# Optimization experiments

Measured on AMD Instinct MI355X. Metric: run time of the kernel, lower is better.

## Reference

```python
import jax, jax.numpy as jnp
import numpy as np

B, S, H = 4, 2048, 1024
E, F = 8, 4096
K = 2  # hardcoded top-k in the original forward


def setup_inputs() -> dict:
    key = jax.random.key(0)
    ks = jax.random.split(key, 8)
    scale = 0.02
    x = jax.random.normal(ks[0], (B, S, H), dtype=jnp.float32)
    Wr = jax.random.normal(ks[1], (H, E), dtype=jnp.float32) * scale
    br = jnp.zeros((E,), dtype=jnp.float32)
    W1 = jax.random.normal(ks[2], (E, H, F), dtype=jnp.float32) * scale
    b1 = jnp.zeros((E, F), dtype=jnp.float32)
    W2 = jax.random.normal(ks[3], (E, F, H), dtype=jnp.float32) * scale
    b2 = jnp.zeros((E, H), dtype=jnp.float32)
    return {"x": x, "Wr": Wr, "br": br, "W1": W1, "b1": b1, "W2": W2, "b2": b2}


def reference(x, Wr, br, W1, b1, W2, b2):
    # Router: [B,S,H] @ [H,E] -> [B,S,E]
    router_logits = jnp.einsum('bsh,he->bse', x, Wr) + br
    router_probs = jax.nn.softmax(router_logits, axis=-1)
    top_k_probs, top_k_indices = jax.lax.top_k(router_probs, K)
    top_k_probs = top_k_probs / jnp.sum(top_k_probs, axis=-1, keepdims=True)
    # NOTE: original code weights EVERY selected expert by the normalized top-1 prob.
    p0 = top_k_probs[..., 0]  # [B,S]

    combined = jnp.zeros((B, S, H), dtype=x.dtype)
    for e in range(E):
        mask = jnp.any(top_k_indices == e, axis=-1)  # [B,S]
        # Dense FFN (dropout deterministic => identity); gelu approximate (flax default)
        h = jax.nn.gelu(jnp.einsum('bsh,hf->bsf', x, W1[e]) + b1[e])
        y = jnp.einsum('bsf,fh->bsh', h, W2[e]) + b2[e]
        combined = combined + jnp.where(mask[..., None], y * p0[..., None], 0.0)
    return combined
```

## Files before the change

### kernel.cpp

```cpp
#include <hip/hip_runtime.h>
#include <hip/hip_bf16.h>


typedef __bf16 bf16;
typedef __attribute__((ext_vector_type(4))) __bf16 bf16x4;
typedef __attribute__((ext_vector_type(8))) __bf16 bf16x8;
typedef __attribute__((ext_vector_type(4))) float f32x4;

#define GLD16(g, l) __builtin_amdgcn_global_load_lds( \
    (__attribute__((address_space(1))) void*)(g),      \
    (__attribute__((address_space(3))) void*)(l), 16, 0, 0)

__device__ __forceinline__ float gelu_fast(float v) {
  float u = v * fmaf(v * v, 0.0713548162726f, 1.5957691216057308f);
  return v * __builtin_amdgcn_rcpf(1.0f + __expf(-u));
}

__global__ __launch_bounds__(256) void router_kernel(
    const float* __restrict__ x, const float* __restrict__ Wr,
    const float* __restrict__ br, int* __restrict__ e01,
    float* __restrict__ p0arr) {
  int wv = threadIdx.x >> 6;
  int l = threadIdx.x & 63;
  int t = blockIdx.x * 4 + wv;
  float acc[8];
#pragma unroll
  for (int e = 0; e < 8; e++) acc[e] = 0.f;
  const float* xr = x + (size_t)t * 1024;
#pragma unroll
  for (int i = 0; i < 16; i++) {
    int h = l + i * 64;
    float xv = xr[h];
    const float4* w4 = (const float4*)(Wr + h * 8);
    float4 wa = w4[0], wb = w4[1];
    acc[0] += xv * wa.x; acc[1] += xv * wa.y; acc[2] += xv * wa.z; acc[3] += xv * wa.w;
    acc[4] += xv * wb.x; acc[5] += xv * wb.y; acc[6] += xv * wb.z; acc[7] += xv * wb.w;
  }
#pragma unroll
  for (int e = 0; e < 8; e++) {
    float v = acc[e];
#pragma unroll
    for (int m = 1; m < 64; m <<= 1) v += __shfl_xor(v, m, 64);
    acc[e] = v + br[e];
  }
  int i1 = 0; float m1 = acc[0];
#pragma unroll
  for (int e = 1; e < 8; e++) { if (acc[e] > m1) { m1 = acc[e]; i1 = e; } }
  int i2 = -1; float m2 = -3.4e38f;
#pragma unroll
  for (int e = 0; e < 8; e++) { if (e != i1 && acc[e] > m2) { m2 = acc[e]; i2 = e; } }
  if (l == 0) {
    e01[t] = i1 | (i2 << 8);
    p0arr[t] = 1.0f / (1.0f + __expf(m2 - m1));
  }
}

__global__ __launch_bounds__(1024) void slots_kernel(
    const int* __restrict__ e01, int* __restrict__ meta,
    int* __restrict__ slot1, int* __restrict__ slot2) {
  __shared__ int wtot[16];
  int tid = threadIdx.x;
  int l = tid & 63, wv = tid >> 6;
  int t0 = tid * 8;
  int i1[8], i2[8];
#pragma unroll
  for (int i = 0; i < 8; i++) {
    int ee = e01[t0 + i];
    i1[i] = ee & 255;
    i2[i] = (ee >> 8) & 255;
  }
  int offl[9];
  int running = 0;
  for (int e = 0; e < 8; e++) {
    offl[e] = running;
    int cthread = 0;
#pragma unroll
    for (int i = 0; i < 8; i++) cthread += (i1[i] == e) + (i2[i] == e);
    int inc = cthread;
#pragma unroll
    for (int d = 1; d < 64; d <<= 1) {
      int v = __shfl_up(inc, d, 64);
      if (l >= d) inc += v;
    }
    if (l == 63) wtot[wv] = inc;
    __syncthreads();
    int wbase = 0, total = 0;
#pragma unroll
    for (int w = 0; w < 16; w++) {
      int tw = wtot[w];
      wbase += (w < wv) ? tw : 0;
      total += tw;
    }
    int base = running + wbase + (inc - cthread);
#pragma unroll
    for (int i = 0; i < 8; i++) {
      if (i1[i] == e) { slot1[t0 + i] = base; base++; }
      if (i2[i] == e) { slot2[t0 + i] = base; base++; }
    }
    running += total;
    __syncthreads();
  }
  offl[8] = running;
  if (tid == 0) {
#pragma unroll
    for (int e = 0; e < 9; e++) meta[e] = offl[e];
    int nt = 0;
    for (int e = 0; e < 8; e++)
      for (int r = offl[e]; r < offl[e + 1]; r += 256)
        meta[16 + (nt++)] = r | (e << 20);
    meta[10] = nt;
  }
}

__global__ __launch_bounds__(256) void gather_kernel(
    const float* __restrict__ x, const int* __restrict__ slot1,
    const int* __restrict__ slot2, bf16* __restrict__ Xg) {
  int t = blockIdx.x;
  int s1 = slot1[t], s2 = slot2[t];
  float4 v = ((const float4*)(x + (size_t)t * 1024))[threadIdx.x];
  bf16x4 bv = { (bf16)v.x, (bf16)v.y, (bf16)v.z, (bf16)v.w };
  *(bf16x4*)(Xg + (size_t)s1 * 1024 + threadIdx.x * 4) = bv;
  *(bf16x4*)(Xg + (size_t)s2 * 1024 + threadIdx.x * 4) = bv;
}

__global__ __launch_bounds__(256) void tconv_kernel(
    const float* __restrict__ in, bf16* __restrict__ out, int R, int C) {
  __shared__ float tile[64][65];
  size_t base = (size_t)blockIdx.z * R * C;
  int gr0 = blockIdx.y * 64, gc0 = blockIdx.x * 64;
#pragma unroll
  for (int i = 0; i < 16; i++) {
    int idx = threadIdx.x + i * 256;
    int r = idx >> 6, c = idx & 63;
    tile[r][c] = in[base + (size_t)(gr0 + r) * C + gc0 + c];
  }
  __syncthreads();
  int rr0 = (threadIdx.x & 15) * 4;
#pragma unroll
  for (int i = 0; i < 4; i++) {
    int cc = (threadIdx.x >> 4) + i * 16;
    bf16x4 v = { (bf16)tile[rr0][cc], (bf16)tile[rr0 + 1][cc],
                 (bf16)tile[rr0 + 2][cc], (bf16)tile[rr0 + 3][cc] };
    *(bf16x4*)&out[base + (size_t)(gc0 + cc) * R + gr0 + rr0] = v;
  }
}

__device__ __forceinline__ void gemm256_core(
    const bf16* __restrict__ Abase, const bf16* __restrict__ Bbase,
    int K, int NT, char* smem, f32x4 acc[8][4], int wr, int wc, int l) {
  int tid = threadIdx.x;
  size_t K2 = (size_t)K * 2;
  const char* src[4];
  int dst[4];
#pragma unroll
  for (int i = 0; i < 4; i++) {
    int s = (i & 1) ? (tid + 512) : tid;
    int byteoff = s * 16;
    int p = byteoff >> 7;
    int W = byteoff & 127;
    int L = W ^ ((p & 7) << 4);
    int r = 2 * p + (L >> 6);
    int c = L & 63;
    const char* base = (const char*)((i >= 2) ? Bbase : Abase);
    src[i] = base + (size_t)r * K2 + c;
    dst[i] = ((i >= 2) ? 16384 : 0) + byteoff;
  }
  int offA[8], offB[4];
  int kc16 = (l >> 4) << 4;
#pragma unroll
  for (int mf = 0; mf < 8; mf++) {
    int r = wr * 128 + mf * 16 + (l & 15);
    int p = r >> 1;
    offA[mf] = (p << 7) + ((((r & 1) << 6) | kc16) ^ ((p & 7) << 4));
  }
#pragma unroll
  for (int nf = 0; nf < 4; nf++) {
    int r = wc * 64 + nf * 16 + (l & 15);
    int p = r >> 1;
    offB[nf] = 16384 + (p << 7) + ((((r & 1) << 6) | kc16) ^ ((p & 7) << 4));
  }
#pragma unroll
  for (int t = 0; t < 3; t++) {
    char* bu = smem + t * 32768;
#pragma unroll
    for (int i = 0; i < 4; i++) GLD16(src[i] + t * 64, bu + dst[i]);
  }
  asm volatile("s_waitcnt vmcnt(8)" ::: "memory");
  __builtin_amdgcn_s_barrier();
  for (int t = 0; t < NT; t++) {
    char* bc = smem + (t & 3) * 32768;
    char* bs = smem + ((t + 3) & 3) * 32768;
    bool st = (t + 3) < NT;
    bf16x8 bfr[4], af[4];
#pragma unroll
    for (int nf = 0; nf < 4; nf++) bfr[nf] = *(const bf16x8*)(bc + offB[nf]);
#pragma unroll
    for (int mf = 0; mf < 4; mf++) af[mf] = *(const bf16x8*)(bc + offA[mf]);
    if (st) {
      GLD16(src[0] + (t + 3) * 64, bs + dst[0]);
      GLD16(src[1] + (t + 3) * 64, bs + dst[1]);
    }
    __builtin_amdgcn_s_barrier();
    asm volatile("s_waitcnt lgkmcnt(0)" ::: "memory");
    __builtin_amdgcn_s_setprio(1);
#pragma unroll
    for (int mf = 0; mf < 4; mf++)
#pragma unroll
      for (int nf = 0; nf < 4; nf++)
        acc[mf][nf] = __builtin_amdgcn_mfma_f32_16x16x32_bf16(bfr[nf], af[mf], acc[mf][nf], 0, 0, 0);
    __builtin_amdgcn_s_setprio(0);
    __builtin_amdgcn_s_barrier();
#pragma unroll
    for (int mf = 0; mf < 4; mf++) af[mf] = *(const bf16x8*)(bc + offA[mf + 4]);
    if (st) {
      GLD16(src[2] + (t + 3) * 64, bs + dst[2]);
      GLD16(src[3] + (t + 3) * 64, bs + dst[3]);
    }
    __builtin_amdgcn_s_barrier();
    asm volatile("s_waitcnt lgkmcnt(0)" ::: "memory");
    __builtin_amdgcn_s_setprio(1);
#pragma unroll
    for (int mf = 0; mf < 4; mf++)
#pragma unroll
      for (int nf = 0; nf < 4; nf++)
        acc[mf + 4][nf] = __builtin_amdgcn_mfma_f32_16x16x32_bf16(bfr[nf], af[mf], acc[mf + 4][nf], 0, 0, 0);
    __builtin_amdgcn_s_setprio(0);
    if ((t + 3) < NT)      { asm volatile("s_waitcnt vmcnt(8)" ::: "memory"); }
    else if ((t + 2) < NT) { asm volatile("s_waitcnt vmcnt(4)" ::: "memory"); }
    else if ((t + 1) < NT) { asm volatile("s_waitcnt vmcnt(0)" ::: "memory"); }
    __builtin_amdgcn_s_barrier();
  }
}

__global__ __launch_bounds__(512, 2) void gemm1_kernel(
    const bf16* __restrict__ Xg, const bf16* __restrict__ W1t,
    const float* __restrict__ b1, bf16* __restrict__ hbuf,
    const int* __restrict__ meta) {
  __shared__ __align__(16) char smem[131072];
  int b = blockIdx.x;
  int xcd = b & 7, j = b >> 3;
  int m_idx = (j >> 4) * 8 + xcd;
  int n_tile = j & 15;
  if (m_idx >= meta[10]) return;
  int ti = meta[16 + m_idx];
  int row0 = ti & 0xFFFFF;
  int e = ti >> 20;
  int rowEnd = meta[1 + e];
  int tid = threadIdx.x;
  int w = tid >> 6, l = tid & 63;
  int wr = w >> 2, wc = w & 3;
  f32x4 acc[8][4];
#pragma unroll
  for (int a = 0; a < 8; a++)
#pragma unroll
    for (int bb = 0; bb < 4; bb++) acc[a][bb] = (f32x4){0.f, 0.f, 0.f, 0.f};
  gemm256_core(Xg + (size_t)row0 * 1024,
               W1t + ((size_t)e * 4096 + n_tile * 256) * 1024,
               1024, 32, smem, acc, wr, wc, l);
  int mrow = l & 15, nq = (l >> 4) * 4;
  int gn0 = n_tile * 256 + wc * 64 + nq;
  f32x4 bv[4];
#pragma unroll
  for (int nf = 0; nf < 4; nf++)
    bv[nf] = *(const f32x4*)(b1 + e * 4096 + gn0 + nf * 16);
#pragma unroll
  for (int mf = 0; mf < 8; mf++) {
    int gm = row0 + wr * 128 + mf * 16 + mrow;
    if (gm < rowEnd) {
      bf16* rp = hbuf + (size_t)gm * 4096 + gn0;
#pragma unroll
      for (int nf = 0; nf < 4; nf++) {
        bf16x4 o;
#pragma unroll
        for (int jj = 0; jj < 4; jj++)
          o[jj] = (bf16)gelu_fast(acc[mf][nf][jj] + bv[nf][jj]);
        *(bf16x4*)(rp + nf * 16) = o;
      }
    }
  }
}

__global__ __launch_bounds__(512, 2) void gemm2_kernel(
    const bf16* __restrict__ hbuf, const bf16* __restrict__ W2t,
    const float* __restrict__ b2, bf16* __restrict__ yb,
    const int* __restrict__ meta) {
  __shared__ __align__(16) char smem[131072];
  int b = blockIdx.x;
  int xcd = b & 7, j = b >> 3;
  int m_idx = (j >> 2) * 8 + xcd;
  int n_tile = j & 3;
  if (m_idx >= meta[10]) return;
  int ti = meta[16 + m_idx];
  int row0 = ti & 0xFFFFF;
  int e = ti >> 20;
  int rowEnd = meta[1 + e];
  int tid = threadIdx.x;
  int w = tid >> 6, l = tid & 63;
  int wr = w >> 2, wc = w & 3;
  f32x4 acc[8][4];
#pragma unroll
  for (int a = 0; a < 8; a++)
#pragma unroll
    for (int bb = 0; bb < 4; bb++) acc[a][bb] = (f32x4){0.f, 0.f, 0.f, 0.f};
  gemm256_core(hbuf + (size_t)row0 * 4096,
               W2t + ((size_t)e * 1024 + n_tile * 256) * 4096,
               4096, 128, smem, acc, wr, wc, l);
  int mrow = l & 15, nq = (l >> 4) * 4;
  int gn0 = n_tile * 256 + wc * 64 + nq;
  f32x4 bv[4];
#pragma unroll
  for (int nf = 0; nf < 4; nf++)
    bv[nf] = *(const f32x4*)(b2 + e * 1024 + gn0 + nf * 16);
#pragma unroll
  for (int mf = 0; mf < 8; mf++) {
    int gm = row0 + wr * 128 + mf * 16 + mrow;
    if (gm < rowEnd) {
      bf16* rp = yb + (size_t)gm * 1024 + gn0;
#pragma unroll
      for (int nf = 0; nf < 4; nf++) {
        bf16x4 o;
#pragma unroll
        for (int jj = 0; jj < 4; jj++)
          o[jj] = (bf16)(acc[mf][nf][jj] + bv[nf][jj]);
        *(bf16x4*)(rp + nf * 16) = o;
      }
    }
  }
}

__global__ __launch_bounds__(256) void combine_kernel(
    const bf16* __restrict__ yb, const int* __restrict__ slot1,
    const int* __restrict__ slot2, const float* __restrict__ p0arr,
    float* __restrict__ out) {
  int t = blockIdx.x;
  int s1 = slot1[t], s2 = slot2[t];
  float w0 = p0arr[t];
  bf16x4 a = *(const bf16x4*)(yb + (size_t)s1 * 1024 + threadIdx.x * 4);
  bf16x4 b = *(const bf16x4*)(yb + (size_t)s2 * 1024 + threadIdx.x * 4);
  float4 o;
  o.x = w0 * ((float)a[0] + (float)b[0]);
  o.y = w0 * ((float)a[1] + (float)b[1]);
  o.z = w0 * ((float)a[2] + (float)b[2]);
  o.w = w0 * ((float)a[3] + (float)b[3]);
  *(float4*)(out + (size_t)t * 1024 + threadIdx.x * 4) = o;
}

extern "C" void kernel_launch(void* const* d_in, const int* in_sizes, int n_in,
                              void* d_out, int out_size, void* d_ws, size_t ws_size,
                              hipStream_t stream) {
  const float* x  = (const float*)d_in[0];
  const float* Wr = (const float*)d_in[1];
  const float* br = (const float*)d_in[2];
  const float* W1 = (const float*)d_in[3];
  const float* b1 = (const float*)d_in[4];
  const float* W2 = (const float*)d_in[5];
  const float* b2 = (const float*)d_in[6];
  float* out = (float*)d_out;

  char* ws = (char*)d_ws;
  int*   meta  = (int*)(ws + 0);
  int*   e01   = (int*)(ws + 4096);
  float* p0    = (float*)(ws + 36864);
  int*   slot1 = (int*)(ws + 69632);
  int*   slot2 = (int*)(ws + 102400);
  bf16*  Xg    = (bf16*)(ws + 135168);
  bf16*  W1t   = (bf16*)(ws + 34213888ULL);
  bf16*  W2t   = (bf16*)(ws + 101322752ULL);
  bf16*  hb    = (bf16*)(ws + 168431616ULL);
  bf16*  yb    = Xg;

  tconv_kernel<<<dim3(64, 16, 8), 256, 0, stream>>>(W1, W1t, 1024, 4096);
  tconv_kernel<<<dim3(16, 64, 8), 256, 0, stream>>>(W2, W2t, 4096, 1024);
  router_kernel<<<2048, 256, 0, stream>>>(x, Wr, br, e01, p0);
  slots_kernel<<<1, 1024, 0, stream>>>(e01, meta, slot1, slot2);
  gather_kernel<<<8192, 256, 0, stream>>>(x, slot1, slot2, Xg);
  gemm1_kernel<<<1152, 512, 0, stream>>>(Xg, W1t, b1, hb, meta);
  gemm2_kernel<<<288, 512, 0, stream>>>(hb, W2t, b2, yb, meta);
  combine_kernel<<<8192, 256, 0, stream>>>(yb, slot1, slot2, p0, out);
}
```

Baseline: 792.6 us.

## Vectorize weight transpose-convert and remap GEMM tiles contiguously per XCD

The fp32-to-bf16 transpose kernel now reads with float4 loads and writes 8-wide bf16 vectors instead of scalar reads and 4-wide writes, which cuts memory instructions. The GEMM block-to-tile mapping also changes. Each XCD now gets a contiguous range of (m,n) tiles, so blocks that share the same A rows and expert weights run on the same XCD and can share its L2, and the count of live tiles is balanced across XCDs. This changes cache locality and load balance but adds a little index arithmetic. If the grid size still assumes the old layout, some blocks may exit early.

```diff
diff --git a/kernel.cpp b/kernel.cpp
--- a/kernel.cpp
+++ b/kernel.cpp
@@ -128,21 +128,40 @@
   __shared__ float tile[64][65];
   size_t base = (size_t)blockIdx.z * R * C;
   int gr0 = blockIdx.y * 64, gc0 = blockIdx.x * 64;
-#pragma unroll
-  for (int i = 0; i < 16; i++) {
-    int idx = threadIdx.x + i * 256;
-    int r = idx >> 6, c = idx & 63;
-    tile[r][c] = in[base + (size_t)(gr0 + r) * C + gc0 + c];
+  int tr = threadIdx.x >> 4;
+  int tc4 = (threadIdx.x & 15) * 4;
+#pragma unroll
+  for (int i = 0; i < 4; i++) {
+    int r = tr + i * 16;
+    float4 v = *(const float4*)&in[base + (size_t)(gr0 + r) * C + gc0 + tc4];
+    tile[r][tc4] = v.x; tile[r][tc4 + 1] = v.y;
+    tile[r][tc4 + 2] = v.z; tile[r][tc4 + 3] = v.w;
   }
   __syncthreads();
-  int rr0 = (threadIdx.x & 15) * 4;
-#pragma unroll
-  for (int i = 0; i < 4; i++) {
-    int cc = (threadIdx.x >> 4) + i * 16;
-    bf16x4 v = { (bf16)tile[rr0][cc], (bf16)tile[rr0 + 1][cc],
-                 (bf16)tile[rr0 + 2][cc], (bf16)tile[rr0 + 3][cc] };
-    *(bf16x4*)&out[base + (size_t)(gc0 + cc) * R + gr0 + rr0] = v;
-  }
+  int rr0 = (threadIdx.x & 7) * 8;
+  int cc0 = threadIdx.x >> 3;
+#pragma unroll
+  for (int i = 0; i < 2; i++) {
+    int cc = cc0 + i * 32;
+    bf16x8 v;
+#pragma unroll
+    for (int k = 0; k < 8; k++) v[k] = (bf16)tile[rr0 + k][cc];
+    *(bf16x8*)&out[base + (size_t)(gc0 + cc) * R + gr0 + rr0] = v;
+  }
+}
+
+__device__ __forceinline__ bool xcd_tile(int b, int ntiles, int nshift,
+                                         int& m_idx, int& n_tile) {
+  int xcd = b & 7, j = b >> 3;
+  int total = ntiles << nshift;
+  int q = total >> 3, r = total & 7;
+  int cnt = q + (xcd < r ? 1 : 0);
+  if (j >= cnt) return false;
+  int start = (xcd < r) ? xcd * (q + 1) : r * (q + 1) + (xcd - r) * q;
+  int tidx = start + j;
+  m_idx = tidx >> nshift;
+  n_tile = tidx & ((1 << nshift) - 1);
+  return true;
 }
 
 __device__ __forceinline__ void gemm256_core(
@@ -237,11 +256,8 @@
     const float* __restrict__ b1, bf16* __restrict__ hbuf,
     const int* __restrict__ meta) {
   __shared__ __align__(16) char smem[131072];
-  int b = blockIdx.x;
-  int xcd = b & 7, j = b >> 3;
-  int m_idx = (j >> 4) * 8 + xcd;
-  int n_tile = j & 15;
-  if (m_idx >= meta[10]) return;
+  int m_idx, n_tile;
+  if (!xcd_tile(blockIdx.x, meta[10], 4, m_idx, n_tile)) return;
   int ti = meta[16 + m_idx];
   int row0 = ti & 0xFFFFF;
   int e = ti >> 20;
@@ -285,11 +301,8 @@
     const float* __restrict__ b2, bf16* __restrict__ yb,
     const int* __restrict__ meta) {
   __shared__ __align__(16) char smem[131072];
-  int b = blockIdx.x;
-  int xcd = b & 7, j = b >> 3;
-  int m_idx = (j >> 2) * 8 + xcd;
-  int n_tile = j & 3;
-  if (m_idx >= meta[10]) return;
+  int m_idx, n_tile;
+  if (!xcd_tile(blockIdx.x, meta[10], 2, m_idx, n_tile)) return;
   int ti = meta[16 + m_idx];
   int row0 = ti & 0xFFFFF;
   int e = ti >> 20;
```

Result: no change. 789.0 us (-0.4%).
